# Kernel optimization log

Hardware: AMD Instinct MI355X
Metric: run time of the kernel (lower is better)

The kernel has to match this reference:

```python
import jax, jax.numpy as jnp
import numpy as np


def _bilinear_sample(fea, px, py):
    # fea: [C,H,W]; px,py: [D,H,W] pixel coords (align_corners=True, zeros padding)
    C, H, W = fea.shape
    x0 = jnp.floor(px); y0 = jnp.floor(py)
    wx = px - x0; wy = py - y0
    x0i = x0.astype(jnp.int32); y0i = y0.astype(jnp.int32)

    def g(xi, yi):
        valid = (xi >= 0) & (xi < W) & (yi >= 0) & (yi < H)
        v = fea[:, jnp.clip(yi, 0, H - 1), jnp.clip(xi, 0, W - 1)]  # [C,D,H,W]
        return jnp.where(valid[None], v, 0.0)

    return (g(x0i, y0i) * ((1 - wx) * (1 - wy))[None]
            + g(x0i + 1, y0i) * (wx * (1 - wy))[None]
            + g(x0i, y0i + 1) * ((1 - wx) * wy)[None]
            + g(x0i + 1, y0i + 1) * (wx * wy)[None])


def homo_warping_3d(src_fea, src_proj, ref_proj, depth_values):
    # src_fea [B,C,H,W]; src_proj/ref_proj [B,4,4]; depth_values [B,D] -> [B,C,D,H,W]
    B, C, H, W = src_fea.shape
    D = depth_values.shape[1]
    proj = src_proj @ jnp.linalg.inv(ref_proj)
    rot, trans = proj[:, :3, :3], proj[:, :3, 3]
    yy, xx = jnp.meshgrid(jnp.arange(H, dtype=src_fea.dtype),
                          jnp.arange(W, dtype=src_fea.dtype), indexing='ij')
    xyz = jnp.stack([xx.ravel(), yy.ravel(), jnp.ones(H * W, src_fea.dtype)], 0)  # [3,HW]
    rot_xyz = jnp.einsum('bij,jp->bip', rot, xyz)  # [B,3,HW]
    pxyz = rot_xyz[:, :, None, :] * depth_values[:, None, :, None] + trans[:, :, None, None]
    xy = pxyz[:, :2] / pxyz[:, 2:3]
    # grid is computed under torch.no_grad() in the original
    px = jax.lax.stop_gradient(xy[:, 0].reshape(B, D, H, W))
    py = jax.lax.stop_gradient(xy[:, 1].reshape(B, D, H, W))
    return jax.vmap(_bilinear_sample)(src_fea, px, py)  # [B,C,D,H,W]


def conf_regression(p, n=4):
    # sliding sum of n consecutive depth probabilities, gathered at expected depth index
    B, D, H, W = p.shape
    pad = jnp.pad(p, ((0, 0), (1, 2), (0, 0), (0, 0)))  # [B,D+3,H,W]
    cs = jnp.cumsum(pad, axis=1)
    cs = jnp.concatenate([jnp.zeros_like(cs[:, :1]), cs], axis=1)  # [B,D+4,H,W]
    sum_n = cs[:, n:n + D] - cs[:, 0:D]  # [B,D,H,W]
    d_idx = jnp.sum(p * jnp.arange(D, dtype=p.dtype)[None, :, None, None], axis=1)
    idx = jnp.clip(d_idx.astype(jnp.int32), 0, D - 1)
    return jnp.take_along_axis(sum_n, idx[:, None], axis=1)[:, 0]


def reference(ref_feats, src_feats, proj_matrices, depth_values, num_depth, w_reg):
    V = proj_matrices.shape[1]
    assert ref_feats.shape[0] == V - 1 and depth_values.shape[1] == num_depth
    ref_proj = proj_matrices[:, 0]
    ref_proj_new = ref_proj[:, 0].at[:, :3, :4].set(ref_proj[:, 1, :3, :3] @ ref_proj[:, 0, :3, :4])
    volume_sum = 0.0
    for v in range(V - 1):
        src_proj = proj_matrices[:, v + 1]
        src_proj_new = src_proj[:, 0].at[:, :3, :4].set(src_proj[:, 1, :3, :3] @ src_proj[:, 0, :3, :4])
        warped = homo_warping_3d(src_feats[v], src_proj_new, ref_proj_new, depth_values)
        volume_sum = volume_sum + ref_feats[v][:, :, None] * warped  # [B,C,D,H,W]
    volume_mean = volume_sum / (V - 1)
    # cost regularization: bias-free 3x3x3 3D conv C->1
    cost = jax.lax.conv_general_dilated(volume_mean, w_reg, (1, 1, 1), 'SAME',
                                        dimension_numbers=('NCDHW', 'OIDHW', 'NCDHW'))
    prob_volume = jax.nn.softmax(cost[:, 0], axis=1)  # [B,D,H,W]
    depth = jnp.sum(prob_volume * depth_values[:, :, None, None], axis=1)  # [B,H,W]
    conf = jax.lax.stop_gradient(conf_regression(prob_volume))  # [B,H,W]
    return depth, conf


def setup_inputs() -> dict:
    key = jax.random.key(0)
    B, V, C, D, H, W = 1, 5, 32, 48, 128, 160
    k1, k2, k3 = jax.random.split(key, 3)
    ref_feats = jax.random.normal(k1, (V - 1, B, C, H, W), jnp.float32)
    src_feats = jax.random.normal(k2, (V - 1, B, C, H, W), jnp.float32)
    # geometrically valid cameras: index 0 = extrinsic 4x4, index 1 = intrinsic 4x4
    f = 200.0
    K = np.eye(4, dtype=np.float32)
    K[0, 0] = f; K[1, 1] = f; K[0, 2] = W / 2.0; K[1, 2] = H / 2.0
    projs = np.zeros((B, V, 2, 4, 4), np.float32)
    for v in range(V):
        ang = 0.04 * v
        R = np.array([[np.cos(ang), 0, np.sin(ang)], [0, 1, 0], [-np.sin(ang), 0, np.cos(ang)]], np.float32)
        E = np.eye(4, dtype=np.float32)
        E[:3, :3] = R
        E[:3, 3] = np.array([-40.0 * v, 0.0, 0.0], np.float32)
        projs[:, v, 0] = E
        projs[:, v, 1] = K
    depth_values = jnp.broadcast_to(jnp.linspace(425.0, 935.0, D, dtype=jnp.float32)[None], (B, D))
    w_reg = jax.random.normal(k3, (1, C, 3, 3, 3), jnp.float32) * 0.05
    return {"ref_feats": ref_feats, "src_feats": src_feats,
            "proj_matrices": jnp.asarray(projs), "depth_values": depth_values,
            "num_depth": D, "w_reg": w_reg}
```

## Files before the change

### kernel.cpp

```cpp
#include <hip/hip_runtime.h>
#include <math.h>

#define H_ 128
#define W_ 160
#define D_ 48
#define C_ 32
#define K27 27
#define HW_ (H_ * W_)
#define DHW_ (D_ * HW_)
#define CHW_ (C_ * HW_)

typedef float f4 __attribute__((ext_vector_type(4)));

__device__ __forceinline__ void build_proj(const float* __restrict__ P, int v,
                                           double M[4][4]) {
    const float* E = P + (v * 2 + 0) * 16;
    const float* K = P + (v * 2 + 1) * 16;
    for (int i = 0; i < 3; i++)
        for (int j = 0; j < 4; j++) {
            double s = 0.0;
            for (int k = 0; k < 3; k++) s += (double)K[i * 4 + k] * (double)E[k * 4 + j];
            M[i][j] = s;
        }
    for (int j = 0; j < 4; j++) M[3][j] = (double)E[12 + j];
}

__global__ void proj_kernel(const float* __restrict__ P, float* __restrict__ rt) {
    if (threadIdx.x != 0) return;
    double M0[4][4];
    build_proj(P, 0, M0);
    double a[4][8];
    for (int i = 0; i < 4; i++)
        for (int j = 0; j < 4; j++) {
            a[i][j] = M0[i][j];
            a[i][4 + j] = (i == j) ? 1.0 : 0.0;
        }
    for (int col = 0; col < 4; ++col) {
        int piv = col;
        double best = fabs(a[col][col]);
        for (int r = col + 1; r < 4; r++) {
            double vv = fabs(a[r][col]);
            if (vv > best) { best = vv; piv = r; }
        }
        if (piv != col)
            for (int j = 0; j < 8; j++) {
                double t = a[col][j]; a[col][j] = a[piv][j]; a[piv][j] = t;
            }
        double inv = 1.0 / a[col][col];
        for (int j = 0; j < 8; j++) a[col][j] *= inv;
        for (int r = 0; r < 4; r++)
            if (r != col) {
                double f = a[r][col];
                for (int j = 0; j < 8; j++) a[r][j] -= f * a[col][j];
            }
    }
    double Minv[4][4];
    for (int i = 0; i < 4; i++)
        for (int j = 0; j < 4; j++) Minv[i][j] = a[i][4 + j];

    for (int v = 1; v < 5; ++v) {
        double Mv[4][4];
        build_proj(P, v, Mv);
        double Pm[4][4];
        for (int i = 0; i < 4; i++)
            for (int j = 0; j < 4; j++) {
                double s = 0.0;
                for (int k = 0; k < 4; k++) s += Mv[i][k] * Minv[k][j];
                Pm[i][j] = s;
            }
        float* o = rt + (v - 1) * 12;
        o[0] = (float)Pm[0][0]; o[1] = (float)Pm[0][1]; o[2] = (float)Pm[0][2];
        o[3] = (float)Pm[1][0]; o[4] = (float)Pm[1][1]; o[5] = (float)Pm[1][2];
        o[6] = (float)Pm[2][0]; o[7] = (float)Pm[2][1]; o[8] = (float)Pm[2][2];
        o[9] = (float)Pm[0][3]; o[10] = (float)Pm[1][3]; o[11] = (float)Pm[2][3];
    }
}

__global__ void transpose_kernel(const float* __restrict__ in,
                                 float* __restrict__ out) {
    int t = blockIdx.x * blockDim.x + threadIdx.x;
    if (t >= 4 * HW_) return;
    int pix = t % HW_;
    int v = t / HW_;
    float vals[C_];
#pragma unroll
    for (int c = 0; c < C_; c++) vals[c] = in[(size_t)v * CHW_ + c * HW_ + pix];
    f4* o = (f4*)(out + ((size_t)v * HW_ + pix) * C_);
#pragma unroll
    for (int q = 0; q < 8; q++) {
        f4 w = {vals[4 * q], vals[4 * q + 1], vals[4 * q + 2], vals[4 * q + 3]};
        o[q] = w;
    }
}

__global__ void __launch_bounds__(256)
warp_fold_x_kernel(const float* __restrict__ srcT,
                   const float* __restrict__ refT,
                   const float* __restrict__ rt,
                   const float* __restrict__ dvals,
                   const float* __restrict__ wreg,
                   float* __restrict__ Gx) {
    __shared__ float accT[8][64][4];
    __shared__ float gLDS[K27][164];

    int t = threadIdx.x;
    int blk = blockIdx.x;
    int d = blk >> 7;
    int y = blk & 127;
    float depth = dvals[d];
    float yf = (float)y;
    int rowbase = d * HW_ + y * W_;

#pragma unroll 1
    for (int b = 0; b < 3; b++) {
        int vox = t >> 2;
        int cgrp = t & 3;
        int vg = b * 64 + vox;
        int x = vg - 1;

        f4 acc0 = (f4){0.f, 0.f, 0.f, 0.f};
        f4 acc1 = (f4){0.f, 0.f, 0.f, 0.f};

        if (x >= 0 && x < W_) {
            float xf = (float)x;
            int pix = y * W_ + x;
#pragma unroll 2
            for (int v = 0; v < 4; v++) {
                const float* m = rt + v * 12;
                float px = fmaf(fmaf(m[0], xf, fmaf(m[1], yf, m[2])), depth, m[9]);
                float py = fmaf(fmaf(m[3], xf, fmaf(m[4], yf, m[5])), depth, m[10]);
                float pz = fmaf(fmaf(m[6], xf, fmaf(m[7], yf, m[8])), depth, m[11]);
                float iz = 1.f / pz;
                px *= iz;
                py *= iz;
                float x0f = floorf(px), y0f = floorf(py);
                float wx = px - x0f, wy = py - y0f;
                int x0 = (int)x0f, y0 = (int)y0f;
                int x1 = x0 + 1, y1 = y0 + 1;

                float w00 = (1.f - wx) * (1.f - wy);
                float w10 = wx * (1.f - wy);
                float w01 = (1.f - wx) * wy;
                float w11 = wx * wy;
                bool vx0 = (x0 >= 0) && (x0 < W_);
                bool vx1 = (x1 >= 0) && (x1 < W_);
                bool vy0 = (y0 >= 0) && (y0 < H_);
                bool vy1 = (y1 >= 0) && (y1 < H_);
                if (!(vx0 && vy0)) w00 = 0.f;
                if (!(vx1 && vy0)) w10 = 0.f;
                if (!(vx0 && vy1)) w01 = 0.f;
                if (!(vx1 && vy1)) w11 = 0.f;
                int cx0 = min(max(x0, 0), W_ - 1);
                int cx1 = min(max(x1, 0), W_ - 1);
                int cy0 = min(max(y0, 0), H_ - 1);
                int cy1 = min(max(y1, 0), H_ - 1);

                const f4* p00 = (const f4*)(srcT + ((size_t)v * HW_ + cy0 * W_ + cx0) * C_ + cgrp * 8);
                const f4* p10 = (const f4*)(srcT + ((size_t)v * HW_ + cy0 * W_ + cx1) * C_ + cgrp * 8);
                const f4* p01 = (const f4*)(srcT + ((size_t)v * HW_ + cy1 * W_ + cx0) * C_ + cgrp * 8);
                const f4* p11 = (const f4*)(srcT + ((size_t)v * HW_ + cy1 * W_ + cx1) * C_ + cgrp * 8);
                const f4* pr  = (const f4*)(refT + ((size_t)v * HW_ + pix) * C_ + cgrp * 8);

                f4 a00 = p00[0], b00 = p00[1];
                f4 a10 = p10[0], b10 = p10[1];
                f4 a01 = p01[0], b01 = p01[1];
                f4 a11 = p11[0], b11 = p11[1];
                f4 r0 = pr[0],  r1 = pr[1];

                f4 sv0 = a00 * w00 + a10 * w10 + a01 * w01 + a11 * w11;
                f4 sv1 = b00 * w00 + b10 * w10 + b01 * w01 + b11 * w11;
                acc0 += r0 * sv0;
                acc1 += r1 * sv1;
            }
            acc0 *= 0.25f;
            acc1 *= 0.25f;
        }

        int cq0 = cgrp * 2;
        *(f4*)&accT[cq0][vox][0] = acc0;
        *(f4*)&accT[cq0 + 1][vox][0] = acc1;
        __syncthreads();

        int fvox = t & 63;
        int kg = t >> 6;
        int fvg = b * 64 + fvox;
        float av[C_];
#pragma unroll
        for (int cq = 0; cq < 8; cq++)
            *(f4*)&av[cq * 4] = *(const f4*)&accT[cq][fvox][0];

        if (fvg < 162) {
            int kstart = kg * 7;
            int kend = min(kstart + 7, K27);
#pragma unroll 1
            for (int k = kstart; k < kend; k++) {
                int ku = __builtin_amdgcn_readfirstlane(k);
                float g = 0.f;
#pragma unroll
                for (int c = 0; c < C_; c++) g = fmaf(wreg[c * K27 + ku], av[c], g);
                gLDS[ku][fvg] = g;
            }
        }
        __syncthreads();
    }

    if (t < W_) {
        int x = t;
#pragma unroll
        for (int j = 0; j < 9; j++) {
            float s = gLDS[j * 3 + 0][x] + gLDS[j * 3 + 1][x + 1] +
                      gLDS[j * 3 + 2][x + 2];
            Gx[(size_t)j * DHW_ + rowbase + x] = s;
        }
    }
}

__global__ void gather9_kernel(const float* __restrict__ Gx,
                               float* __restrict__ cost) {
    int t = blockIdx.x * blockDim.x + threadIdx.x;
    if (t >= DHW_ / 4) return;
    int idx = t * 4;
    int x = idx % W_;
    int y = (idx / W_) % H_;
    int d = idx / HW_;
    f4 acc = (f4){0.f, 0.f, 0.f, 0.f};
#pragma unroll
    for (int kd = 0; kd < 3; kd++) {
        int dd = d + kd - 1;
        if ((unsigned)dd >= (unsigned)D_) continue;
#pragma unroll
        for (int kh = 0; kh < 3; kh++) {
            int yy = y + kh - 1;
            if ((unsigned)yy >= (unsigned)H_) continue;
            int j = kd * 3 + kh;
            acc += *(const f4*)(Gx + (size_t)j * DHW_ + dd * HW_ + yy * W_ + x);
        }
    }
    *(f4*)(cost + idx) = acc;
}

__global__ void softmax_kernel(const float* __restrict__ cost,
                               const float* __restrict__ dvals,
                               float* __restrict__ out) {
    int pix = blockIdx.x * blockDim.x + threadIdx.x;
    if (pix >= HW_) return;
    float mx = -1e30f;
#pragma unroll 1
    for (int d = 0; d < D_; d++) mx = fmaxf(mx, cost[d * HW_ + pix]);
    float s = 0.f, dnum = 0.f, inum = 0.f;
#pragma unroll 1
    for (int d = 0; d < D_; d++) {
        float e = __expf(cost[d * HW_ + pix] - mx);
        s += e;
        dnum = fmaf(e, dvals[d], dnum);
        inum = fmaf(e, (float)d, inum);
    }
    float invs = 1.f / s;
    float depth = dnum * invs;
    float didx = inum * invs;
    int id = (int)didx;
    id = min(max(id, 0), D_ - 1);
    float conf = 0.f;
    for (int k = id - 1; k <= id + 2; ++k)
        if (k >= 0 && k < D_) conf += __expf(cost[k * HW_ + pix] - mx);
    conf *= invs;
    out[pix] = depth;
    out[HW_ + pix] = conf;
}

extern "C" void kernel_launch(void* const* d_in, const int* in_sizes, int n_in,
                              void* d_out, int out_size, void* d_ws, size_t ws_size,
                              hipStream_t stream) {
    const float* ref_feats = (const float*)d_in[0];
    const float* src_feats = (const float*)d_in[1];
    const float* proj      = (const float*)d_in[2];
    const float* dvals     = (const float*)d_in[3];
    const float* wreg      = (const float*)d_in[5];
    float* out = (float*)d_out;

    char* ws = (char*)d_ws;
    float* rt   = (float*)ws;
    float* srcT = (float*)(ws + 1024);
    float* refT = srcT + (size_t)4 * HW_ * C_;
    float* Gx   = refT + (size_t)4 * HW_ * C_;
    float* cost = Gx + (size_t)9 * DHW_;

    proj_kernel<<<1, 64, 0, stream>>>(proj, rt);
    transpose_kernel<<<(4 * HW_) / 256, 256, 0, stream>>>(src_feats, srcT);
    transpose_kernel<<<(4 * HW_) / 256, 256, 0, stream>>>(ref_feats, refT);
    warp_fold_x_kernel<<<D_ * H_, 256, 0, stream>>>(srcT, refT, rt, dvals, wreg, Gx);
    gather9_kernel<<<(DHW_ / 4) / 256, 256, 0, stream>>>(Gx, cost);
    softmax_kernel<<<HW_ / 256, 256, 0, stream>>>(cost, dvals, out);
}
```

Measured before the change: 217.2 us.

## Fuse depth/height gather with softmax regression and merge transpose launches

Replaces the separate gather9 and softmax kernels with one kernel per row tile. It sums the nine partial-conv planes for 12 depths per thread group, then does a shared-memory max/sum reduction and the confidence lookup, so the full cost volume is never written and re-read. The two transpose launches are merged into one, and the per-row projection terms are hoisted out of the x loop in the warp kernel. The fused kernel launches only 384 blocks and reads Gx without vectorized loads, which may lower occupancy and bandwidth use.

Result: slower. 251.2 us (+15.7%).

```diff
diff --git a/kernel.cpp b/kernel.cpp
--- a/kernel.cpp
+++ b/kernel.cpp
@@ -76,10 +76,18 @@
     }
 }
 
-__global__ void transpose_kernel(const float* __restrict__ in,
-                                 float* __restrict__ out) {
+__global__ void transpose2_kernel(const float* __restrict__ sf,
+                                  const float* __restrict__ rf,
+                                  float* __restrict__ so,
+                                  float* __restrict__ ro) {
     int t = blockIdx.x * blockDim.x + threadIdx.x;
-    if (t >= 4 * HW_) return;
+    const float* in = sf;
+    float* out = so;
+    if (t >= 4 * HW_) {
+        t -= 4 * HW_;
+        in = rf;
+        out = ro;
+    }
     int pix = t % HW_;
     int v = t / HW_;
     float vals[C_];
@@ -104,6 +112,8 @@
     __shared__ float gLDS[K27][164];
 
     int t = threadIdx.x;
+    int vox = t >> 2;
+    int cgrp = t & 3;
     int blk = blockIdx.x;
     int d = blk >> 7;
     int y = blk & 127;
@@ -111,10 +121,20 @@
     float yf = (float)y;
     int rowbase = d * HW_ + y * W_;
 
+    float Ax[4], Bx[4], Ay[4], By[4], Az[4], Bz[4];
+#pragma unroll
+    for (int v = 0; v < 4; v++) {
+        const float* m = rt + v * 12;
+        Ax[v] = fmaf(fmaf(m[1], yf, m[2]), depth, m[9]);
+        Bx[v] = m[0] * depth;
+        Ay[v] = fmaf(fmaf(m[4], yf, m[5]), depth, m[10]);
+        By[v] = m[3] * depth;
+        Az[v] = fmaf(fmaf(m[7], yf, m[8]), depth, m[11]);
+        Bz[v] = m[6] * depth;
+    }
+
 #pragma unroll 1
     for (int b = 0; b < 3; b++) {
-        int vox = t >> 2;
-        int cgrp = t & 3;
         int vg = b * 64 + vox;
         int x = vg - 1;
 
@@ -126,13 +146,10 @@
             int pix = y * W_ + x;
 #pragma unroll 2
             for (int v = 0; v < 4; v++) {
-                const float* m = rt + v * 12;
-                float px = fmaf(fmaf(m[0], xf, fmaf(m[1], yf, m[2])), depth, m[9]);
-                float py = fmaf(fmaf(m[3], xf, fmaf(m[4], yf, m[5])), depth, m[10]);
-                float pz = fmaf(fmaf(m[6], xf, fmaf(m[7], yf, m[8])), depth, m[11]);
+                float pz = fmaf(Bz[v], xf, Az[v]);
                 float iz = 1.f / pz;
-                px *= iz;
-                py *= iz;
+                float px = fmaf(Bx[v], xf, Ax[v]) * iz;
+                float py = fmaf(By[v], xf, Ay[v]) * iz;
                 float x0f = floorf(px), y0f = floorf(py);
                 float wx = px - x0f, wy = py - y0f;
                 int x0 = (int)x0f, y0 = (int)y0f;
@@ -155,10 +172,11 @@
                 int cy0 = min(max(y0, 0), H_ - 1);
                 int cy1 = min(max(y1, 0), H_ - 1);
 
-                const f4* p00 = (const f4*)(srcT + ((size_t)v * HW_ + cy0 * W_ + cx0) * C_ + cgrp * 8);
-                const f4* p10 = (const f4*)(srcT + ((size_t)v * HW_ + cy0 * W_ + cx1) * C_ + cgrp * 8);
-                const f4* p01 = (const f4*)(srcT + ((size_t)v * HW_ + cy1 * W_ + cx0) * C_ + cgrp * 8);
-                const f4* p11 = (const f4*)(srcT + ((size_t)v * HW_ + cy1 * W_ + cx1) * C_ + cgrp * 8);
+                const float* sv = srcT + (size_t)v * HW_ * C_ + cgrp * 8;
+                const f4* p00 = (const f4*)(sv + (cy0 * W_ + cx0) * C_);
+                const f4* p10 = (const f4*)(sv + (cy0 * W_ + cx1) * C_);
+                const f4* p01 = (const f4*)(sv + (cy1 * W_ + cx0) * C_);
+                const f4* p11 = (const f4*)(sv + (cy1 * W_ + cx1) * C_);
                 const f4* pr  = (const f4*)(refT + ((size_t)v * HW_ + pix) * C_ + cgrp * 8);
 
                 f4 a00 = p00[0], b00 = p00[1];
@@ -215,57 +233,89 @@
     }
 }
 
-__global__ void gather9_kernel(const float* __restrict__ Gx,
-                               float* __restrict__ cost) {
-    int t = blockIdx.x * blockDim.x + threadIdx.x;
-    if (t >= DHW_ / 4) return;
-    int idx = t * 4;
-    int x = idx % W_;
-    int y = (idx / W_) % H_;
-    int d = idx / HW_;
-    f4 acc = (f4){0.f, 0.f, 0.f, 0.f};
-#pragma unroll
-    for (int kd = 0; kd < 3; kd++) {
-        int dd = d + kd - 1;
-        if ((unsigned)dd >= (unsigned)D_) continue;
-#pragma unroll
-        for (int kh = 0; kh < 3; kh++) {
-            int yy = y + kh - 1;
-            if ((unsigned)yy >= (unsigned)H_) continue;
-            int j = kd * 3 + kh;
-            acc += *(const f4*)(Gx + (size_t)j * DHW_ + dd * HW_ + yy * W_ + x);
-        }
-    }
-    *(f4*)(cost + idx) = acc;
-}
-
-__global__ void softmax_kernel(const float* __restrict__ cost,
-                               const float* __restrict__ dvals,
-                               float* __restrict__ out) {
-    int pix = blockIdx.x * blockDim.x + threadIdx.x;
-    if (pix >= HW_) return;
-    float mx = -1e30f;
+__global__ void __launch_bounds__(256)
+gather_softmax_kernel(const float* __restrict__ Gx,
+                      const float* __restrict__ dvals,
+                      float* __restrict__ out) {
+    __shared__ float E[D_][64];
+    __shared__ float red[4][64];
+    __shared__ float sums[3][4][64];
+
+    int t = threadIdx.x;
+    int lx = t & 63;
+    int dg = t >> 6;
+    int blk = blockIdx.x;
+    int xt = blk % 3;
+    int y = blk / 3;
+    int x = xt * 64 + lx;
+    bool xv = x < W_;
+    int xc = min(x, W_ - 1);
+    int dbase = dg * 12 - 1;
+
+    float S0[14], S1[14], S2[14];
+#pragma unroll
+    for (int jj = 0; jj < 14; jj++) {
+        float s0 = 0.f, s1 = 0.f, s2 = 0.f;
+        int dp = dbase + jj;
+        if ((unsigned)dp < (unsigned)D_) {
+            const float* g0 = Gx + (size_t)dp * HW_ + xc;
+#pragma unroll
+            for (int kh = 0; kh < 3; kh++) {
+                int yy = y + kh - 1;
+                if ((unsigned)yy < (unsigned)H_) {
+                    const float* gp = g0 + yy * W_ + (size_t)kh * DHW_;
+                    s0 += gp[0];
+                    s1 += *(gp + (size_t)3 * DHW_);
+                    s2 += *(gp + (size_t)6 * DHW_);
+                }
+            }
+        }
+        S0[jj] = s0; S1[jj] = s1; S2[jj] = s2;
+    }
+
+    float cost[12];
+    float lmax = -1e30f;
+#pragma unroll
+    for (int j = 0; j < 12; j++) {
+        cost[j] = S0[j] + S1[j + 1] + S2[j + 2];
+        lmax = fmaxf(lmax, cost[j]);
+    }
+    red[dg][lx] = lmax;
+    __syncthreads();
+    float mx = fmaxf(fmaxf(red[0][lx], red[1][lx]),
+                     fmaxf(red[2][lx], red[3][lx]));
+
+    float s = 0.f, dn = 0.f, din = 0.f;
+#pragma unroll
+    for (int j = 0; j < 12; j++) {
+        int dd = dg * 12 + j;
+        float e = __expf(cost[j] - mx);
+        E[dd][lx] = e;
+        s += e;
+        dn = fmaf(e, dvals[dd], dn);
+        din = fmaf(e, (float)dd, din);
+    }
+    sums[0][dg][lx] = s;
+    sums[1][dg][lx] = dn;
+    sums[2][dg][lx] = din;
+    __syncthreads();
+
+    if (dg == 0 && xv) {
+        float S = sums[0][0][lx] + sums[0][1][lx] + sums[0][2][lx] + sums[0][3][lx];
+        float DN = sums[1][0][lx] + sums[1][1][lx] + sums[1][2][lx] + sums[1][3][lx];
+        float DI = sums[2][0][lx] + sums[2][1][lx] + sums[2][2][lx] + sums[2][3][lx];
+        float invs = 1.f / S;
+        float depth = DN * invs;
+        int id = (int)(DI * invs);
+        id = min(max(id, 0), D_ - 1);
+        float conf = 0.f;
 #pragma unroll 1
-    for (int d = 0; d < D_; d++) mx = fmaxf(mx, cost[d * HW_ + pix]);
-    float s = 0.f, dnum = 0.f, inum = 0.f;
-#pragma unroll 1
-    for (int d = 0; d < D_; d++) {
-        float e = __expf(cost[d * HW_ + pix] - mx);
-        s += e;
-        dnum = fmaf(e, dvals[d], dnum);
-        inum = fmaf(e, (float)d, inum);
-    }
-    float invs = 1.f / s;
-    float depth = dnum * invs;
-    float didx = inum * invs;
-    int id = (int)didx;
-    id = min(max(id, 0), D_ - 1);
-    float conf = 0.f;
-    for (int k = id - 1; k <= id + 2; ++k)
-        if (k >= 0 && k < D_) conf += __expf(cost[k * HW_ + pix] - mx);
-    conf *= invs;
-    out[pix] = depth;
-    out[HW_ + pix] = conf;
+        for (int k = id - 1; k <= id + 2; ++k)
+            if (k >= 0 && k < D_) conf += E[k][lx];
+        int pix = y * W_ + x;
+        out[pix] = depth;
+        out[HW_ + pix] = conf * invs;
+    }
 }
 
 extern "C" void kernel_launch(void* const* d_in, const int* in_sizes, int n_in,
@@ -283,12 +333,10 @@
     float* srcT = (float*)(ws + 1024);
     float* refT = srcT + (size_t)4 * HW_ * C_;
     float* Gx   = refT + (size_t)4 * HW_ * C_;
-    float* cost = Gx + (size_t)9 * DHW_;
 
     proj_kernel<<<1, 64, 0, stream>>>(proj, rt);
-    transpose_kernel<<<(4 * HW_) / 256, 256, 0, stream>>>(src_feats, srcT);
-    transpose_kernel<<<(4 * HW_) / 256, 256, 0, stream>>>(ref_feats, refT);
+    transpose2_kernel<<<(8 * HW_) / 256, 256, 0, stream>>>(src_feats, ref_feats,
+                                                           srcT, refT);
     warp_fold_x_kernel<<<D_ * H_, 256, 0, stream>>>(srcT, refT, rt, dvals, wreg, Gx);
-    gather9_kernel<<<(DHW_ / 4) / 256, 256, 0, stream>>>(Gx, cost);
-    softmax_kernel<<<HW_ / 256, 256, 0, stream>>>(cost, dvals, out);
-}
+    gather_softmax_kernel<<<3 * H_, 256, 0, stream>>>(Gx, dvals, out);
+}
```
